# Kernel optimization log

Measured on AMD Instinct MI355X. Metric: run time of the kernel, lower is better.

Reference implementation:

```python
import jax, jax.numpy as jnp
import numpy as np

K = 8            # kernel volume = down_ratio^3 = 2^3
N_IN = 40000     # coarse (input) active voxels
N_OUT = 150000   # fine (output/skip) active voxels
C_IN = 128
C_EMB = 128
C_SKIP = 128
EPS = 1e-5


def setup_inputs() -> dict:
    key = jax.random.key(0)
    ks = jax.random.split(key, 8)
    x_feat = jax.random.normal(ks[0], (N_IN, C_IN), dtype=jnp.float32)
    skip_feat = jax.random.normal(ks[1], (N_OUT, C_SKIP), dtype=jnp.float32)
    pair_in = jax.random.randint(ks[2], (K, N_OUT), 0, N_IN, dtype=jnp.int32)
    pair_out = jax.random.randint(ks[3], (K, N_OUT), 0, N_OUT, dtype=jnp.int32)
    W_up = jax.random.normal(ks[4], (K, C_IN, C_EMB), dtype=jnp.float32) * 0.02
    W1 = jax.random.normal(ks[5], (C_SKIP + C_EMB, C_EMB), dtype=jnp.float32) * 0.05
    W2 = jax.random.normal(ks[6], (C_EMB, C_EMB), dtype=jnp.float32) * 0.05
    return {
        "x_feat": x_feat, "skip_feat": skip_feat,
        "pair_in": pair_in, "pair_out": pair_out,
        "W_up": W_up,
        "g0": jnp.ones((C_EMB,), jnp.float32), "b0": jnp.zeros((C_EMB,), jnp.float32),
        "W1": W1, "b1": jnp.zeros((C_EMB,), jnp.float32),
        "g1": jnp.ones((C_EMB,), jnp.float32), "be1": jnp.zeros((C_EMB,), jnp.float32),
        "W2": W2, "b2": jnp.zeros((C_EMB,), jnp.float32),
        "g2": jnp.ones((C_EMB,), jnp.float32), "be2": jnp.zeros((C_EMB,), jnp.float32),
    }


def _bn(x, gamma, beta):
    # BatchNorm1d over the point axis (training-mode batch stats, biased var)
    m = jnp.mean(x, axis=0)
    v = jnp.mean(jnp.square(x - m), axis=0)
    return (x - m) * jax.lax.rsqrt(v + EPS) * gamma + beta


def reference(x_feat, skip_feat, pair_in, pair_out, W_up,
              g0, b0, W1, b1, g1, be1, W2, b2, g2, be2):
    n_out = skip_feat.shape[0]
    # SparseInverseConv3d: gather coarse features, per-offset GEMM, scatter-add
    out = jnp.zeros((n_out, W_up.shape[2]), dtype=x_feat.dtype)
    for k in range(K):  # fixed small kernel volume, structurally distinct weights
        contrib = x_feat[pair_in[k]] @ W_up[k]          # [P, C_emb]
        out = out.at[pair_out[k]].add(contrib)
    up = jax.nn.relu(_bn(out, g0, b0))                  # [N_out, C_emb]

    # fuse: concat([up, skip]) -> Linear/BN/ReLU x2, residual with up
    h = jnp.concatenate([up, skip_feat], axis=1)        # [N_out, C_emb+C_skip]
    h = jax.nn.relu(_bn(h @ W1 + b1, g1, be1))
    h = jax.nn.relu(_bn(h @ W2 + b2, g2, be2))
    return h + up
```

## Files before the change

kernel.cpp:

```cpp
#include <hip/hip_runtime.h>

#define KVOL 8
#define NIN 40000
#define NOUT 150000
#define C 128
#define EPSV 1e-5f
#define NPAIR (KVOL * NOUT)
#define GM ((NOUT + 63) / 64)
#define GM2 ((NOUT + 127) / 128)
#define GUP (NIN / 64)
#define BROWS 64
#define NBUCK ((NOUT + BROWS - 1) / BROWS)
#define NSTR 8
#define SCAP 128
#define BCAP (NSTR * SCAP)
#define GBUCK ((NPAIR + 4095) / 4096)

typedef __attribute__((ext_vector_type(8))) __bf16 bf16x8;
typedef __attribute__((ext_vector_type(4))) float f32x4;
typedef __attribute__((ext_vector_type(8))) unsigned short us8;

__device__ __forceinline__ unsigned short fbf(float f) {
    unsigned u = __float_as_uint(f);
    u += 0x7fffu + ((u >> 16) & 1u);
    return (unsigned short)(u >> 16);
}
__device__ __forceinline__ float bff(unsigned short s) {
    return __uint_as_float(((unsigned)s) << 16);
}

__global__ __launch_bounds__(256) void k_prep_w(
    const float* __restrict__ Wup, const float* __restrict__ W1, const float* __restrict__ W2,
    unsigned short* __restrict__ WT)
{
    int i = blockIdx.x * 256 + threadIdx.x;
    if (i < 11 * 16384) {
        int b = i >> 14, r = i & 16383;
        int k = r >> 7, n = r & 127;
        const float* src = (b < 8) ? (Wup + (size_t)b * 16384)
                         : (b < 10) ? (W1 + (size_t)(b - 8) * 16384) : W2;
        WT[(size_t)b * 16384 + n * 128 + k] = fbf(src[k * 128 + n]);
    }
}

__global__ __launch_bounds__(256) void k_bucket2(
    const int* __restrict__ pout, const int* __restrict__ pin,
    int* __restrict__ bcnt, unsigned int* __restrict__ bbuf)
{
    __shared__ int cnt[NBUCK];
    __shared__ int bas[NBUCK];
    __shared__ int run[NBUCK];
    const int t = threadIdx.x;
    const int str = blockIdx.x & (NSTR - 1);
    const int i0 = blockIdx.x * 4096;
    for (int b = t; b < NBUCK; b += 256) { cnt[b] = 0; run[b] = 0; }
    __syncthreads();
    for (int j = t; j < 4096; j += 256) {
        int i = i0 + j;
        if (i < NPAIR) atomicAdd(&cnt[pout[i] >> 6], 1);
    }
    __syncthreads();
    for (int b = t; b < NBUCK; b += 256) {
        int c = cnt[b];
        bas[b] = c ? atomicAdd(&bcnt[str * NBUCK + b], c) : 0;
    }
    __syncthreads();
    for (int j = t; j < 4096; j += 256) {
        int i = i0 + j;
        if (i < NPAIR) {
            int o = pout[i];
            int k = i / NOUT;
            unsigned e = (unsigned)(k * NIN + pin[i]);
            int b = o >> 6;
            int dst = bas[b] + atomicAdd(&run[b], 1);
            if (dst < SCAP)
                bbuf[((size_t)str * NBUCK + b) * SCAP + dst] = ((unsigned)(o & 63) << 24) | e;
        }
    }
}

__global__ __launch_bounds__(256) void k_up(
    const float* __restrict__ x, const unsigned short* __restrict__ WT,
    unsigned short* __restrict__ Y)
{
    __shared__ __align__(16) unsigned short Alds[64][136];
    __shared__ __align__(16) unsigned short Wlds[128][136];
    const int t = threadIdx.x;
    const int wave = t >> 6, lane = t & 63;
    const int l15 = lane & 15, lhi = lane >> 4;
    const int R = blockIdx.x * 64;
    const float4* A4 = (const float4*)x;
    #pragma unroll
    for (int j = 0; j < 8; ++j) {
        int idx = t + j * 256;
        int row = idx >> 5, c4 = idx & 31;
        int grow = R + row;
        float4 v = make_float4(0.f, 0.f, 0.f, 0.f);
        if (grow < NIN) v = A4[(size_t)grow * 32 + c4];
        ushort4 o;
        o.x = fbf(v.x); o.y = fbf(v.y); o.z = fbf(v.z); o.w = fbf(v.w);
        *(ushort4*)&Alds[row][c4 * 4] = o;
    }
    __syncthreads();
    bf16x8 af[4];
    #pragma unroll
    for (int kk = 0; kk < 4; ++kk)
        af[kk] = *(const bf16x8*)&Alds[wave * 16 + l15][kk * 32 + lhi * 8];
    unsigned short* scr = (unsigned short*)&Wlds[0][0];
    for (int k = 0; k < KVOL; ++k) {
        __syncthreads();
        const us8* Wsrc = (const us8*)(WT + (size_t)k * C * C);
        #pragma unroll
        for (int j = 0; j < 8; ++j) {
            int slot = t + j * 256;
            int n = slot >> 4, koff = (slot & 15) * 8;
            *(us8*)&Wlds[n][koff] = Wsrc[slot];
        }
        __syncthreads();
        f32x4 acc[8];
        #pragma unroll
        for (int n = 0; n < 8; ++n) acc[n] = (f32x4){0.f, 0.f, 0.f, 0.f};
        #pragma unroll
        for (int n = 0; n < 8; ++n) {
            #pragma unroll
            for (int kk = 0; kk < 4; ++kk) {
                bf16x8 bfr = *(const bf16x8*)&Wlds[n * 16 + l15][kk * 32 + lhi * 8];
                acc[n] = __builtin_amdgcn_mfma_f32_16x16x32_bf16(af[kk], bfr, acc[n], 0, 0, 0);
            }
        }
        __syncthreads();
        #pragma unroll
        for (int n = 0; n < 8; ++n) {
            const int col = n * 16 + l15;
            #pragma unroll
            for (int r = 0; r < 4; ++r)
                scr[(wave * 16 + lhi * 4 + r) * 136 + col] = fbf(acc[n][r]);
        }
        __syncthreads();
        us8* Yk8 = (us8*)(Y + (size_t)k * NIN * C);
        #pragma unroll
        for (int j = 0; j < 4; ++j) {
            int slot = t + j * 256;
            int lrow = slot >> 4, c8 = slot & 15;
            Yk8[(size_t)(R + lrow) * 16 + c8] = *(const us8*)&scr[lrow * 136 + c8 * 8];
        }
    }
}

template<int PHASES, bool BNIN, bool STATS>
__global__ __launch_bounds__(512) void k_mfma(
    const void* __restrict__ A0v, const void* __restrict__ A1v,
    const unsigned short* __restrict__ WT,
    const float* __restrict__ bias,
    unsigned short* __restrict__ outp, int M,
    const float* __restrict__ bn_stats, const float* __restrict__ bn_g, const float* __restrict__ bn_b,
    float* __restrict__ parts)
{
    __shared__ __align__(16) unsigned short Alds[128][136];
    __shared__ __align__(16) unsigned short Wlds[128][136];
    __shared__ float sscale[C], sshift[C];
    const int t = threadIdx.x;
    const int wave = t >> 6, lane = t & 63;
    const int l15 = lane & 15, lhi = lane >> 4;
    const int R = blockIdx.x * 128;

    if (BNIN) {
        if (t < C) {
            float m = bn_stats[t] * (1.0f / NOUT);
            float var = bn_stats[C + t] * (1.0f / NOUT) - m * m;
            float sc = bn_g[t] * rsqrtf(var + EPSV);
            sscale[t] = sc;
            sshift[t] = fmaf(-m, sc, bn_b[t]);
        }
        __syncthreads();
    }

    f32x4 acc[8];
    #pragma unroll
    for (int n = 0; n < 8; ++n) acc[n] = (f32x4){0.f, 0.f, 0.f, 0.f};

    {
        const us8* Wsrc = (const us8*)WT;
        #pragma unroll
        for (int j = 0; j < 4; ++j) {
            int slot = t + j * 512;
            *(us8*)&Wlds[slot >> 4][(slot & 15) * 8] = Wsrc[slot];
        }
        const us8* A8 = (const us8*)A0v;
        #pragma unroll
        for (int j = 0; j < 4; ++j) {
            int slot = t + j * 512;
            int row = slot >> 4, s15 = slot & 15, koff = s15 * 8;
            int grow = R + row;
            us8 v = (us8){0, 0, 0, 0, 0, 0, 0, 0};
            if (grow < M) v = A8[(size_t)grow * 16 + s15];
            if (BNIN) {
                us8 w;
                #pragma unroll
                for (int i = 0; i < 8; ++i) {
                    float f = fmaxf(fmaf(bff(v[i]), sscale[koff + i], sshift[koff + i]), 0.f);
                    w[i] = fbf(f);
                }
                v = w;
            }
            *(us8*)&Alds[row][koff] = v;
        }
    }
    __syncthreads();

    if constexpr (PHASES == 2) {
        us8 wreg[4];
        float4 areg[8];
        {
            const us8* Wsrc1 = (const us8*)(WT + C * C);
            #pragma unroll
            for (int j = 0; j < 4; ++j) wreg[j] = Wsrc1[t + j * 512];
            const float4* A41 = (const float4*)A1v;
            #pragma unroll
            for (int j = 0; j < 8; ++j) {
                int slot = t + j * 512;
                int row = slot >> 5, c4 = slot & 31;
                int grow = R + row;
                float4 v = make_float4(0.f, 0.f, 0.f, 0.f);
                if (grow < M) v = A41[(size_t)grow * 32 + c4];
                areg[j] = v;
            }
        }
        {
            bf16x8 af[4];
            #pragma unroll
            for (int kk = 0; kk < 4; ++kk)
                af[kk] = *(const bf16x8*)&Alds[wave * 16 + l15][kk * 32 + lhi * 8];
            #pragma unroll
            for (int n = 0; n < 8; ++n) {
                #pragma unroll
                for (int kk = 0; kk < 4; ++kk) {
                    bf16x8 bfr = *(const bf16x8*)&Wlds[n * 16 + l15][kk * 32 + lhi * 8];
                    acc[n] = __builtin_amdgcn_mfma_f32_16x16x32_bf16(af[kk], bfr, acc[n], 0, 0, 0);
                }
            }
        }
        __syncthreads();
        #pragma unroll
        for (int j = 0; j < 4; ++j) {
            int slot = t + j * 512;
            *(us8*)&Wlds[slot >> 4][(slot & 15) * 8] = wreg[j];
        }
        #pragma unroll
        for (int j = 0; j < 8; ++j) {
            int slot = t + j * 512;
            int row = slot >> 5, c4 = slot & 31;
            float4 v = areg[j];
            ushort4 o;
            o.x = fbf(v.x); o.y = fbf(v.y); o.z = fbf(v.z); o.w = fbf(v.w);
            *(ushort4*)&Alds[row][c4 * 4] = o;
        }
        __syncthreads();
    }
    {
        bf16x8 af[4];
        #pragma unroll
        for (int kk = 0; kk < 4; ++kk)
            af[kk] = *(const bf16x8*)&Alds[wave * 16 + l15][kk * 32 + lhi * 8];
        #pragma unroll
        for (int n = 0; n < 8; ++n) {
            #pragma unroll
            for (int kk = 0; kk < 4; ++kk) {
                bf16x8 bfr = *(const bf16x8*)&Wlds[n * 16 + l15][kk * 32 + lhi * 8];
                acc[n] = __builtin_amdgcn_mfma_f32_16x16x32_bf16(af[kk], bfr, acc[n], 0, 0, 0);
            }
        }
    }
    __syncthreads();

    unsigned short* scr = (unsigned short*)&Wlds[0][0];
    float* sbS = (float*)&Alds[0][0];
    float* sbQ = sbS + 1024;
    #pragma unroll
    for (int n = 0; n < 8; ++n) {
        const int col = n * 16 + l15;
        float bv = bias[col];
        float s = 0.f, q = 0.f;
        #pragma unroll
        for (int r = 0; r < 4; ++r) {
            int lrow = wave * 16 + lhi * 4 + r;
            float v = acc[n][r] + bv;
            scr[lrow * 136 + col] = fbf(v);
            if (STATS && (R + lrow) < M) { s += v; q = fmaf(v, v, q); }
        }
        if (STATS) {
            s += __shfl_xor(s, 16); s += __shfl_xor(s, 32);
            q += __shfl_xor(q, 16); q += __shfl_xor(q, 32);
            if (lane < 16) {
                sbS[wave * 128 + col] = s;
                sbQ[wave * 128 + col] = q;
            }
        }
    }
    __syncthreads();
    us8* out8 = (us8*)outp;
    #pragma unroll
    for (int j = 0; j < 4; ++j) {
        int slot = t + j * 512;
        int lrow = slot >> 4, c8 = slot & 15;
        int grow = R + lrow;
        if (grow < M) out8[(size_t)grow * 16 + c8] = *(const us8*)&scr[lrow * 136 + c8 * 8];
    }
    if (STATS) {
        if (t < 128) {
            float S = 0.f;
            #pragma unroll
            for (int w = 0; w < 8; ++w) S += sbS[w * 128 + t];
            parts[(size_t)blockIdx.x * 256 + t] = S;
        } else if (t < 256) {
            int cc = t - 128;
            float Q = 0.f;
            #pragma unroll
            for (int w = 0; w < 8; ++w) Q += sbQ[w * 128 + cc];
            parts[(size_t)blockIdx.x * 256 + t] = Q;
        }
    }
}

__global__ __launch_bounds__(256) void k_reduce(const float* __restrict__ parts, int nb,
                                                float* __restrict__ stats)
{
    const int t = threadIdx.x;
    float s0 = 0.f, s1 = 0.f, s2 = 0.f, s3 = 0.f;
    for (int b = blockIdx.x * 4; b < nb; b += gridDim.x * 4) {
        if (b < nb)     s0 += parts[(size_t)b * 256 + t];
        if (b + 1 < nb) s1 += parts[(size_t)(b + 1) * 256 + t];
        if (b + 2 < nb) s2 += parts[(size_t)(b + 2) * 256 + t];
        if (b + 3 < nb) s3 += parts[(size_t)(b + 3) * 256 + t];
    }
    atomicAdd(&stats[t], (s0 + s1) + (s2 + s3));
}

__global__ __launch_bounds__(256) void k_sortgather(
    const int* __restrict__ bcnt, const unsigned int* __restrict__ bbuf,
    const us8* __restrict__ Y8, us8* __restrict__ up8, float* __restrict__ parts)
{
    __shared__ unsigned int pr[BCAP];
    __shared__ unsigned int srt[BCAP];
    __shared__ int cnt[BROWS], sd[BROWS], ofs2[BROWS];
    const int t = threadIdx.x;
    const int b = blockIdx.x;
    int segbase = 0;
    #pragma unroll
    for (int s = 0; s < NSTR; ++s) {
        int ns = min(bcnt[s * NBUCK + b], SCAP);
        const unsigned int* g = bbuf + ((size_t)s * NBUCK + b) * SCAP;
        for (int j = t; j < ns; j += 256) pr[segbase + j] = g[j];
        segbase += ns;
    }
    const int n = segbase;
    if (t < BROWS) cnt[t] = 0;
    __syncthreads();
    for (int j = t; j < n; j += 256) atomicAdd(&cnt[pr[j] >> 24], 1);
    __syncthreads();
    if (t < BROWS) sd[t] = cnt[t];
    __syncthreads();
    for (int off = 1; off < BROWS; off <<= 1) {
        int a = (t < BROWS) ? sd[t] : 0;
        int bb = (t < BROWS && t >= off) ? sd[t - off] : 0;
        __syncthreads();
        if (t < BROWS) sd[t] = a + bb;
        __syncthreads();
    }
    if (t < BROWS) ofs2[t] = sd[t] - cnt[t];
    __syncthreads();
    for (int j = t; j < n; j += 256) {
        unsigned p = pr[j];
        int pos = atomicAdd(&ofs2[p >> 24], 1);
        srt[pos] = p & 0xFFFFFFu;
    }
    __syncthreads();
    const int wave = t >> 6, lane = t & 63;
    const int rl = t >> 4, c8 = t & 15;
    float s8[8], q8[8];
    #pragma unroll
    for (int i = 0; i < 8; ++i) { s8[i] = 0.f; q8[i] = 0.f; }
    #pragma unroll
    for (int it = 0; it < 4; ++it) {
        int r = it * 16 + rl;
        int o = b * BROWS + r;
        if (o < NOUT) {
            int j1 = sd[r], j0 = j1 - cnt[r];
            float a[8];
            #pragma unroll
            for (int i = 0; i < 8; ++i) a[i] = 0.f;
            int j = j0;
            for (; j + 1 < j1; j += 2) {
                unsigned e0 = srt[j], e1 = srt[j + 1];
                us8 u0 = Y8[(size_t)e0 * 16 + c8];
                us8 u1 = Y8[(size_t)e1 * 16 + c8];
                #pragma unroll
                for (int i = 0; i < 8; ++i) a[i] += bff(u0[i]) + bff(u1[i]);
            }
            if (j < j1) {
                unsigned e0 = srt[j];
                us8 u0 = Y8[(size_t)e0 * 16 + c8];
                #pragma unroll
                for (int i = 0; i < 8; ++i) a[i] += bff(u0[i]);
            }
            us8 o8;
            #pragma unroll
            for (int i = 0; i < 8; ++i) {
                o8[i] = fbf(a[i]);
                s8[i] += a[i];
                q8[i] = fmaf(a[i], a[i], q8[i]);
            }
            up8[(size_t)o * 16 + c8] = o8;
        }
    }
    #pragma unroll
    for (int i = 0; i < 8; ++i) {
        s8[i] += __shfl_xor(s8[i], 16); s8[i] += __shfl_xor(s8[i], 32);
        q8[i] += __shfl_xor(q8[i], 16); q8[i] += __shfl_xor(q8[i], 32);
    }
    float* sS = (float*)pr;
    float* sQ = sS + 512;
    if (lane < 16) {
        #pragma unroll
        for (int i = 0; i < 8; ++i) {
            sS[(wave * 16 + c8) * 8 + i] = s8[i];
            sQ[(wave * 16 + c8) * 8 + i] = q8[i];
        }
    }
    __syncthreads();
    if (t < 128) {
        const int cc = t >> 3, ii = t & 7;
        float S = 0.f, Q = 0.f;
        #pragma unroll
        for (int w = 0; w < 4; ++w) {
            S += sS[(w * 16 + cc) * 8 + ii];
            Q += sQ[(w * 16 + cc) * 8 + ii];
        }
        parts[(size_t)b * 256 + t] = S;
        parts[(size_t)b * 256 + 128 + t] = Q;
    }
}

__global__ __launch_bounds__(256) void k_final(
    const us8* __restrict__ h2, const us8* __restrict__ upr, float* __restrict__ out,
    const float* __restrict__ stats2, const float* __restrict__ g2, const float* __restrict__ be2,
    const float* __restrict__ stats0, const float* __restrict__ g0, const float* __restrict__ b0)
{
    __shared__ float sc2[C], sh2[C], sc0[C], sh0[C];
    const int t = threadIdx.x;
    if (t < C) {
        float m2 = stats2[t] * (1.0f / NOUT);
        float v2 = stats2[C + t] * (1.0f / NOUT) - m2 * m2;
        float c2 = g2[t] * rsqrtf(v2 + EPSV);
        sc2[t] = c2; sh2[t] = fmaf(-m2, c2, be2[t]);
        float m0 = stats0[t] * (1.0f / NOUT);
        float v0 = stats0[C + t] * (1.0f / NOUT) - m0 * m0;
        float c0 = g0[t] * rsqrtf(v0 + EPSV);
        sc0[t] = c0; sh0[t] = fmaf(-m0, c0, b0[t]);
    }
    __syncthreads();
    const int idx0 = blockIdx.x * 256 + t;
    const int c8 = idx0 & 15;
    float l2s[8], l2h[8], l0s[8], l0h[8];
    #pragma unroll
    for (int i = 0; i < 8; ++i) {
        l2s[i] = sc2[c8 * 8 + i]; l2h[i] = sh2[c8 * 8 + i];
        l0s[i] = sc0[c8 * 8 + i]; l0h[i] = sh0[c8 * 8 + i];
    }
    const int total = NOUT * 16;
    for (int idx = idx0; idx < total; idx += gridDim.x * 256) {
        us8 h = h2[idx];
        us8 u = upr[idx];
        float o[8];
        #pragma unroll
        for (int i = 0; i < 8; ++i) {
            o[i] = fmaxf(fmaf(bff(h[i]), l2s[i], l2h[i]), 0.f)
                 + fmaxf(fmaf(bff(u[i]), l0s[i], l0h[i]), 0.f);
        }
        float4* dst = (float4*)&out[(size_t)idx * 8];
        dst[0] = make_float4(o[0], o[1], o[2], o[3]);
        dst[1] = make_float4(o[4], o[5], o[6], o[7]);
    }
}

extern "C" void kernel_launch(void* const* d_in, const int* in_sizes, int n_in,
                              void* d_out, int out_size, void* d_ws, size_t ws_size,
                              hipStream_t stream)
{
    const float* x    = (const float*)d_in[0];
    const float* skip = (const float*)d_in[1];
    const int*   pin  = (const int*)d_in[2];
    const int*   pout = (const int*)d_in[3];
    const float* Wup  = (const float*)d_in[4];
    const float* g0   = (const float*)d_in[5];
    const float* b0   = (const float*)d_in[6];
    const float* W1   = (const float*)d_in[7];
    const float* b1   = (const float*)d_in[8];
    const float* g1   = (const float*)d_in[9];
    const float* be1  = (const float*)d_in[10];
    const float* W2   = (const float*)d_in[11];
    const float* b2   = (const float*)d_in[12];
    const float* g2   = (const float*)d_in[13];
    const float* be2  = (const float*)d_in[14];
    float* outp = (float*)d_out;

    char* base = (char*)d_ws;
    unsigned short* Y      = (unsigned short*)base;
    unsigned short* h1     = (unsigned short*)base;
    unsigned short* h2     = (unsigned short*)(base + 40960000);
    unsigned short* up_raw = (unsigned short*)(base + 81920000);
    char* p = base + 81920000 + 38400000;
    unsigned short* WT = (unsigned short*)p; p += (size_t)11 * 16384 * 2;
    unsigned int* bbuf = (unsigned int*)p;  p += (size_t)NSTR * NBUCK * SCAP * 4;
    int* bcnt      = (int*)p; p += (size_t)NSTR * NBUCK * 4;
    float* parts0  = (float*)p; p += (size_t)NBUCK * 256 * 4;
    float* parts1  = (float*)p; p += (size_t)GM * 256 * 4;
    float* parts2  = (float*)p; p += (size_t)GM * 256 * 4;
    float* stats   = (float*)p; p += 3 * 256 * 4;

    hipMemsetAsync(bcnt, 0, (size_t)NSTR * NBUCK * 4, stream);
    hipMemsetAsync(stats, 0, 3 * 256 * 4, stream);

    k_prep_w<<<(11 * 16384 + 255) / 256, 256, 0, stream>>>(Wup, W1, W2, WT);

    k_bucket2<<<GBUCK, 256, 0, stream>>>(pout, pin, bcnt, bbuf);

    k_up<<<GUP, 256, 0, stream>>>(x, WT, Y);

    k_sortgather<<<NBUCK, 256, 0, stream>>>(bcnt, bbuf, (const us8*)Y, (us8*)up_raw, parts0);
    k_reduce<<<16, 256, 0, stream>>>(parts0, NBUCK, stats);

    k_mfma<2, true, true><<<GM2, 512, 0, stream>>>(
        up_raw, skip, WT + (size_t)8 * 16384, b1, h1, NOUT, stats, g0, b0, parts1);
    k_reduce<<<16, 256, 0, stream>>>(parts1, GM2, stats + 256);

    k_mfma<1, true, true><<<GM2, 512, 0, stream>>>(
        h1, nullptr, WT + (size_t)10 * 16384, b2, h2, NOUT, stats + 256, g1, be1, parts2);
    k_reduce<<<16, 256, 0, stream>>>(parts2, GM2, stats + 512);

    k_final<<<1024, 256, 0, stream>>>((const us8*)h2, (const us8*)up_raw, outp,
        stats + 512, g2, be2, stats, g0, b0);
}
```

Baseline: 330.2 us.

## Make GEMM kernels persistent with resident weights and direct register-loaded A operands

k_up now launches one grid dimension per kernel offset, loads that offset's weight slice into LDS once, and loops over row tiles. It loads x directly from global memory into MFMA fragments instead of staging through LDS. The k_mfma kernels become persistent grids (512 and 768 blocks) that keep both weight phases resident in LDS, build A fragments straight from global memory with the BN+ReLU applied in registers, and accumulate BN statistics across tiles in registers. This removes per-tile weight reloads and several barriers, but the outputs are now written as scattered 2-byte stores instead of coalesced 16-byte rows, and the A loads are less coalesced.

```diff
diff --git a/kernel.cpp b/kernel.cpp
--- a/kernel.cpp
+++ b/kernel.cpp
@@ -7,8 +7,9 @@
 #define EPSV 1e-5f
 #define NPAIR (KVOL * NOUT)
 #define GM ((NOUT + 63) / 64)
-#define GM2 ((NOUT + 127) / 128)
 #define GUP (NIN / 64)
+#define GUPX 105
+#define NT128 ((NOUT + 127) / 128)
 #define BROWS 64
 #define NBUCK ((NOUT + BROWS - 1) / BROWS)
 #define NSTR 8
@@ -83,40 +84,32 @@
     const float* __restrict__ x, const unsigned short* __restrict__ WT,
     unsigned short* __restrict__ Y)
 {
-    __shared__ __align__(16) unsigned short Alds[64][136];
-    __shared__ __align__(16) unsigned short Wlds[128][136];
+    __shared__ __align__(16) unsigned short Wlds[128 * 136];
     const int t = threadIdx.x;
     const int wave = t >> 6, lane = t & 63;
     const int l15 = lane & 15, lhi = lane >> 4;
-    const int R = blockIdx.x * 64;
-    const float4* A4 = (const float4*)x;
+    const int k = blockIdx.y;
+    const us8* Wsrc = (const us8*)(WT + (size_t)k * C * C);
     #pragma unroll
     for (int j = 0; j < 8; ++j) {
-        int idx = t + j * 256;
-        int row = idx >> 5, c4 = idx & 31;
-        int grow = R + row;
-        float4 v = make_float4(0.f, 0.f, 0.f, 0.f);
-        if (grow < NIN) v = A4[(size_t)grow * 32 + c4];
-        ushort4 o;
-        o.x = fbf(v.x); o.y = fbf(v.y); o.z = fbf(v.z); o.w = fbf(v.w);
-        *(ushort4*)&Alds[row][c4 * 4] = o;
-    }
-    __syncthreads();
-    bf16x8 af[4];
-    #pragma unroll
-    for (int kk = 0; kk < 4; ++kk)
-        af[kk] = *(const bf16x8*)&Alds[wave * 16 + l15][kk * 32 + lhi * 8];
-    unsigned short* scr = (unsigned short*)&Wlds[0][0];
-    for (int k = 0; k < KVOL; ++k) {
-        __syncthreads();
-        const us8* Wsrc = (const us8*)(WT + (size_t)k * C * C);
-        #pragma unroll
-        for (int j = 0; j < 8; ++j) {
-            int slot = t + j * 256;
-            int n = slot >> 4, koff = (slot & 15) * 8;
-            *(us8*)&Wlds[n][koff] = Wsrc[slot];
-        }
-        __syncthreads();
+        int slot = t + j * 256;
+        *(us8*)&Wlds[(slot >> 4) * 136 + (slot & 15) * 8] = Wsrc[slot];
+    }
+    __syncthreads();
+    unsigned short* Yk = Y + (size_t)k * NIN * C;
+    for (int tile = blockIdx.x; tile < GUP; tile += GUPX) {
+        const int R = tile * 64;
+        const int row = R + wave * 16 + l15;
+        bf16x8 af[4];
+        #pragma unroll
+        for (int kk = 0; kk < 4; ++kk) {
+            float4 v0 = *(const float4*)&x[(size_t)row * C + kk * 32 + lhi * 8];
+            float4 v1 = *(const float4*)&x[(size_t)row * C + kk * 32 + lhi * 8 + 4];
+            union { us8 u; bf16x8 b; } cv;
+            cv.u[0] = fbf(v0.x); cv.u[1] = fbf(v0.y); cv.u[2] = fbf(v0.z); cv.u[3] = fbf(v0.w);
+            cv.u[4] = fbf(v1.x); cv.u[5] = fbf(v1.y); cv.u[6] = fbf(v1.z); cv.u[7] = fbf(v1.w);
+            af[kk] = cv.b;
+        }
         f32x4 acc[8];
         #pragma unroll
         for (int n = 0; n < 8; ++n) acc[n] = (f32x4){0.f, 0.f, 0.f, 0.f};
@@ -124,30 +117,23 @@
         for (int n = 0; n < 8; ++n) {
             #pragma unroll
             for (int kk = 0; kk < 4; ++kk) {
-                bf16x8 bfr = *(const bf16x8*)&Wlds[n * 16 + l15][kk * 32 + lhi * 8];
+                bf16x8 bfr = *(const bf16x8*)&Wlds[(n * 16 + l15) * 136 + kk * 32 + lhi * 8];
                 acc[n] = __builtin_amdgcn_mfma_f32_16x16x32_bf16(af[kk], bfr, acc[n], 0, 0, 0);
             }
         }
-        __syncthreads();
         #pragma unroll
         for (int n = 0; n < 8; ++n) {
             const int col = n * 16 + l15;
             #pragma unroll
-            for (int r = 0; r < 4; ++r)
-                scr[(wave * 16 + lhi * 4 + r) * 136 + col] = fbf(acc[n][r]);
-        }
-        __syncthreads();
-        us8* Yk8 = (us8*)(Y + (size_t)k * NIN * C);
-        #pragma unroll
-        for (int j = 0; j < 4; ++j) {
-            int slot = t + j * 256;
-            int lrow = slot >> 4, c8 = slot & 15;
-            Yk8[(size_t)(R + lrow) * 16 + c8] = *(const us8*)&scr[lrow * 136 + c8 * 8];
-        }
-    }
-}
-
-template<int PHASES, bool BNIN, bool STATS>
+            for (int r = 0; r < 4; ++r) {
+                int orow = R + wave * 16 + lhi * 4 + r;
+                Yk[(size_t)orow * C + col] = fbf(acc[n][r]);
+            }
+        }
+    }
+}
+
+template<int PHASES, bool BNIN, bool STATS, int PGRID>
 __global__ __launch_bounds__(512) void k_mfma(
     const void* __restrict__ A0v, const void* __restrict__ A1v,
     const unsigned short* __restrict__ WT,
@@ -156,167 +142,144 @@
     const float* __restrict__ bn_stats, const float* __restrict__ bn_g, const float* __restrict__ bn_b,
     float* __restrict__ parts)
 {
-    __shared__ __align__(16) unsigned short Alds[128][136];
-    __shared__ __align__(16) unsigned short Wlds[128][136];
+    __shared__ __align__(16) unsigned short Wlds[PHASES * 128 * 136];
     __shared__ float sscale[C], sshift[C];
+    __shared__ float sb[2 * 8 * 128];
     const int t = threadIdx.x;
     const int wave = t >> 6, lane = t & 63;
     const int l15 = lane & 15, lhi = lane >> 4;
-    const int R = blockIdx.x * 128;
-
-    if (BNIN) {
-        if (t < C) {
-            float m = bn_stats[t] * (1.0f / NOUT);
-            float var = bn_stats[C + t] * (1.0f / NOUT) - m * m;
-            float sc = bn_g[t] * rsqrtf(var + EPSV);
-            sscale[t] = sc;
-            sshift[t] = fmaf(-m, sc, bn_b[t]);
-        }
-        __syncthreads();
-    }
-
-    f32x4 acc[8];
-    #pragma unroll
-    for (int n = 0; n < 8; ++n) acc[n] = (f32x4){0.f, 0.f, 0.f, 0.f};
-
+
+    if (BNIN && t < C) {
+        float m = bn_stats[t] * (1.0f / NOUT);
+        float var = bn_stats[C + t] * (1.0f / NOUT) - m * m;
+        float sc = bn_g[t] * rsqrtf(var + EPSV);
+        sscale[t] = sc;
+        sshift[t] = fmaf(-m, sc, bn_b[t]);
+    }
     {
         const us8* Wsrc = (const us8*)WT;
         #pragma unroll
-        for (int j = 0; j < 4; ++j) {
+        for (int j = 0; j < 4 * PHASES; ++j) {
             int slot = t + j * 512;
-            *(us8*)&Wlds[slot >> 4][(slot & 15) * 8] = Wsrc[slot];
-        }
-        const us8* A8 = (const us8*)A0v;
-        #pragma unroll
-        for (int j = 0; j < 4; ++j) {
-            int slot = t + j * 512;
-            int row = slot >> 4, s15 = slot & 15, koff = s15 * 8;
-            int grow = R + row;
-            us8 v = (us8){0, 0, 0, 0, 0, 0, 0, 0};
-            if (grow < M) v = A8[(size_t)grow * 16 + s15];
-            if (BNIN) {
-                us8 w;
-                #pragma unroll
-                for (int i = 0; i < 8; ++i) {
-                    float f = fmaxf(fmaf(bff(v[i]), sscale[koff + i], sshift[koff + i]), 0.f);
-                    w[i] = fbf(f);
-                }
-                v = w;
-            }
-            *(us8*)&Alds[row][koff] = v;
-        }
-    }
-    __syncthreads();
-
-    if constexpr (PHASES == 2) {
-        us8 wreg[4];
-        float4 areg[8];
-        {
-            const us8* Wsrc1 = (const us8*)(WT + C * C);
-            #pragma unroll
-            for (int j = 0; j < 4; ++j) wreg[j] = Wsrc1[t + j * 512];
-            const float4* A41 = (const float4*)A1v;
-            #pragma unroll
-            for (int j = 0; j < 8; ++j) {
-                int slot = t + j * 512;
-                int row = slot >> 5, c4 = slot & 31;
-                int grow = R + row;
-                float4 v = make_float4(0.f, 0.f, 0.f, 0.f);
-                if (grow < M) v = A41[(size_t)grow * 32 + c4];
-                areg[j] = v;
-            }
-        }
+            int ph = slot >> 11;
+            int rr = (slot >> 4) & 127;
+            *(us8*)&Wlds[(ph * 128 + rr) * 136 + (slot & 15) * 8] = Wsrc[slot];
+        }
+    }
+    __syncthreads();
+
+    float bv[8];
+    #pragma unroll
+    for (int n = 0; n < 8; ++n) bv[n] = bias[n * 16 + l15];
+    float sAcc[8], qAcc[8];
+    #pragma unroll
+    for (int n = 0; n < 8; ++n) { sAcc[n] = 0.f; qAcc[n] = 0.f; }
+
+    const us8* A8 = (const us8*)A0v;
+    const float* A1f = (const float*)A1v;
+
+    for (int tile = blockIdx.x; tile < NT128; tile += PGRID) {
+        const int R = tile * 128;
+        const int row = R + wave * 16 + l15;
+        const bool ok = row < M;
+        f32x4 acc[8];
+        #pragma unroll
+        for (int n = 0; n < 8; ++n) acc[n] = (f32x4){0.f, 0.f, 0.f, 0.f};
         {
             bf16x8 af[4];
             #pragma unroll
-            for (int kk = 0; kk < 4; ++kk)
-                af[kk] = *(const bf16x8*)&Alds[wave * 16 + l15][kk * 32 + lhi * 8];
+            for (int kk = 0; kk < 4; ++kk) {
+                us8 v = (us8){0, 0, 0, 0, 0, 0, 0, 0};
+                if (ok) v = A8[(size_t)row * 16 + kk * 4 + lhi];
+                union { us8 u; bf16x8 b; } cv;
+                if (BNIN) {
+                    const float4 s0 = *(const float4*)&sscale[kk * 32 + lhi * 8];
+                    const float4 s1 = *(const float4*)&sscale[kk * 32 + lhi * 8 + 4];
+                    const float4 h0 = *(const float4*)&sshift[kk * 32 + lhi * 8];
+                    const float4 h1 = *(const float4*)&sshift[kk * 32 + lhi * 8 + 4];
+                    cv.u[0] = fbf(fmaxf(fmaf(bff(v[0]), s0.x, h0.x), 0.f));
+                    cv.u[1] = fbf(fmaxf(fmaf(bff(v[1]), s0.y, h0.y), 0.f));
+                    cv.u[2] = fbf(fmaxf(fmaf(bff(v[2]), s0.z, h0.z), 0.f));
+                    cv.u[3] = fbf(fmaxf(fmaf(bff(v[3]), s0.w, h0.w), 0.f));
+                    cv.u[4] = fbf(fmaxf(fmaf(bff(v[4]), s1.x, h1.x), 0.f));
+                    cv.u[5] = fbf(fmaxf(fmaf(bff(v[5]), s1.y, h1.y), 0.f));
+                    cv.u[6] = fbf(fmaxf(fmaf(bff(v[6]), s1.z, h1.z), 0.f));
+                    cv.u[7] = fbf(fmaxf(fmaf(bff(v[7]), s1.w, h1.w), 0.f));
+                } else {
+                    cv.u = v;
+                }
+                af[kk] = cv.b;
+            }
             #pragma unroll
             for (int n = 0; n < 8; ++n) {
                 #pragma unroll
                 for (int kk = 0; kk < 4; ++kk) {
-                    bf16x8 bfr = *(const bf16x8*)&Wlds[n * 16 + l15][kk * 32 + lhi * 8];
+                    bf16x8 bfr = *(const bf16x8*)&Wlds[(n * 16 + l15) * 136 + kk * 32 + lhi * 8];
                     acc[n] = __builtin_amdgcn_mfma_f32_16x16x32_bf16(af[kk], bfr, acc[n], 0, 0, 0);
                 }
             }
         }
+        if constexpr (PHASES == 2) {
+            bf16x8 af[4];
+            #pragma unroll
+            for (int kk = 0; kk < 4; ++kk) {
+                float4 v0 = make_float4(0.f, 0.f, 0.f, 0.f), v1 = v0;
+                if (ok) {
+                    v0 = *(const float4*)&A1f[(size_t)row * C + kk * 32 + lhi * 8];
+                    v1 = *(const float4*)&A1f[(size_t)row * C + kk * 32 + lhi * 8 + 4];
+                }
+                union { us8 u; bf16x8 b; } cv;
+                cv.u[0] = fbf(v0.x); cv.u[1] = fbf(v0.y); cv.u[2] = fbf(v0.z); cv.u[3] = fbf(v0.w);
+                cv.u[4] = fbf(v1.x); cv.u[5] = fbf(v1.y); cv.u[6] = fbf(v1.z); cv.u[7] = fbf(v1.w);
+                af[kk] = cv.b;
+            }
+            #pragma unroll
+            for (int n = 0; n < 8; ++n) {
+                #pragma unroll
+                for (int kk = 0; kk < 4; ++kk) {
+                    bf16x8 bfr = *(const bf16x8*)&Wlds[(128 + n * 16 + l15) * 136 + kk * 32 + lhi * 8];
+                    acc[n] = __builtin_amdgcn_mfma_f32_16x16x32_bf16(af[kk], bfr, acc[n], 0, 0, 0);
+                }
+            }
+        }
+        #pragma unroll
+        for (int n = 0; n < 8; ++n) {
+            const int col = n * 16 + l15;
+            #pragma unroll
+            for (int r = 0; r < 4; ++r) {
+                int orow = R + wave * 16 + lhi * 4 + r;
+                if (orow < M) {
+                    float v = acc[n][r] + bv[n];
+                    outp[(size_t)orow * C + col] = fbf(v);
+                    if (STATS) { sAcc[n] += v; qAcc[n] = fmaf(v, v, qAcc[n]); }
+                }
+            }
+        }
+    }
+    if (STATS) {
+        #pragma unroll
+        for (int n = 0; n < 8; ++n) {
+            sAcc[n] += __shfl_xor(sAcc[n], 16); sAcc[n] += __shfl_xor(sAcc[n], 32);
+            qAcc[n] += __shfl_xor(qAcc[n], 16); qAcc[n] += __shfl_xor(qAcc[n], 32);
+        }
+        if (lane < 16) {
+            #pragma unroll
+            for (int n = 0; n < 8; ++n) {
+                sb[wave * 128 + n * 16 + l15] = sAcc[n];
+                sb[1024 + wave * 128 + n * 16 + l15] = qAcc[n];
+            }
+        }
         __syncthreads();
-        #pragma unroll
-        for (int j = 0; j < 4; ++j) {
-            int slot = t + j * 512;
-            *(us8*)&Wlds[slot >> 4][(slot & 15) * 8] = wreg[j];
-        }
-        #pragma unroll
-        for (int j = 0; j < 8; ++j) {
-            int slot = t + j * 512;
-            int row = slot >> 5, c4 = slot & 31;
-            float4 v = areg[j];
-            ushort4 o;
-            o.x = fbf(v.x); o.y = fbf(v.y); o.z = fbf(v.z); o.w = fbf(v.w);
-            *(ushort4*)&Alds[row][c4 * 4] = o;
-        }
-        __syncthreads();
-    }
-    {
-        bf16x8 af[4];
-        #pragma unroll
-        for (int kk = 0; kk < 4; ++kk)
-            af[kk] = *(const bf16x8*)&Alds[wave * 16 + l15][kk * 32 + lhi * 8];
-        #pragma unroll
-        for (int n = 0; n < 8; ++n) {
-            #pragma unroll
-            for (int kk = 0; kk < 4; ++kk) {
-                bf16x8 bfr = *(const bf16x8*)&Wlds[n * 16 + l15][kk * 32 + lhi * 8];
-                acc[n] = __builtin_amdgcn_mfma_f32_16x16x32_bf16(af[kk], bfr, acc[n], 0, 0, 0);
-            }
-        }
-    }
-    __syncthreads();
-
-    unsigned short* scr = (unsigned short*)&Wlds[0][0];
-    float* sbS = (float*)&Alds[0][0];
-    float* sbQ = sbS + 1024;
-    #pragma unroll
-    for (int n = 0; n < 8; ++n) {
-        const int col = n * 16 + l15;
-        float bv = bias[col];
-        float s = 0.f, q = 0.f;
-        #pragma unroll
-        for (int r = 0; r < 4; ++r) {
-            int lrow = wave * 16 + lhi * 4 + r;
-            float v = acc[n][r] + bv;
-            scr[lrow * 136 + col] = fbf(v);
-            if (STATS && (R + lrow) < M) { s += v; q = fmaf(v, v, q); }
-        }
-        if (STATS) {
-            s += __shfl_xor(s, 16); s += __shfl_xor(s, 32);
-            q += __shfl_xor(q, 16); q += __shfl_xor(q, 32);
-            if (lane < 16) {
-                sbS[wave * 128 + col] = s;
-                sbQ[wave * 128 + col] = q;
-            }
-        }
-    }
-    __syncthreads();
-    us8* out8 = (us8*)outp;
-    #pragma unroll
-    for (int j = 0; j < 4; ++j) {
-        int slot = t + j * 512;
-        int lrow = slot >> 4, c8 = slot & 15;
-        int grow = R + lrow;
-        if (grow < M) out8[(size_t)grow * 16 + c8] = *(const us8*)&scr[lrow * 136 + c8 * 8];
-    }
-    if (STATS) {
         if (t < 128) {
             float S = 0.f;
             #pragma unroll
-            for (int w = 0; w < 8; ++w) S += sbS[w * 128 + t];
+            for (int w = 0; w < 8; ++w) S += sb[w * 128 + t];
             parts[(size_t)blockIdx.x * 256 + t] = S;
         } else if (t < 256) {
             int cc = t - 128;
             float Q = 0.f;
             #pragma unroll
-            for (int w = 0; w < 8; ++w) Q += sbQ[w * 128 + cc];
+            for (int w = 0; w < 8; ++w) Q += sb[1024 + w * 128 + cc];
             parts[(size_t)blockIdx.x * 256 + t] = Q;
         }
     }
@@ -525,18 +488,18 @@
 
     k_bucket2<<<GBUCK, 256, 0, stream>>>(pout, pin, bcnt, bbuf);
 
-    k_up<<<GUP, 256, 0, stream>>>(x, WT, Y);
+    k_up<<<dim3(GUPX, KVOL), 256, 0, stream>>>(x, WT, Y);
 
     k_sortgather<<<NBUCK, 256, 0, stream>>>(bcnt, bbuf, (const us8*)Y, (us8*)up_raw, parts0);
     k_reduce<<<16, 256, 0, stream>>>(parts0, NBUCK, stats);
 
-    k_mfma<2, true, true><<<GM2, 512, 0, stream>>>(
+    k_mfma<2, true, true, 512><<<512, 512, 0, stream>>>(
         up_raw, skip, WT + (size_t)8 * 16384, b1, h1, NOUT, stats, g0, b0, parts1);
-    k_reduce<<<16, 256, 0, stream>>>(parts1, GM2, stats + 256);
-
-    k_mfma<1, true, true><<<GM2, 512, 0, stream>>>(
+    k_reduce<<<16, 256, 0, stream>>>(parts1, 512, stats + 256);
+
+    k_mfma<1, true, true, 768><<<768, 512, 0, stream>>>(
         h1, nullptr, WT + (size_t)10 * 16384, b2, h2, NOUT, stats + 256, g1, be1, parts2);
-    k_reduce<<<16, 256, 0, stream>>>(parts2, GM2, stats + 512);
+    k_reduce<<<16, 256, 0, stream>>>(parts2, 768, stats + 512);
 
     k_final<<<1024, 256, 0, stream>>>((const us8*)h2, (const us8*)up_raw, outp,
         stats + 512, g2, be2, stats, g0, b0);
```

After: 432.9 us. 1.31x slower.
